# Kernel optimization log

Hardware: AMD Instinct MI355X
Metric: run time of the kernel (lower is better)

Reference implementation:

```python
import math
import jax, jax.numpy as jnp
import numpy as np

B, N, D, Pd, L, H = 2, 384, 256, 64, 8, 8
Dh = D // H
VOCAB = 21


def _layernorm(x, w, b, eps=1e-5):
    m = jnp.mean(x, axis=-1, keepdims=True)
    v = jnp.var(x, axis=-1, keepdims=True)
    return (x - m) * jax.lax.rsqrt(v + eps) * w + b


def _safe_norm(v):
    return jnp.sqrt(jnp.sum(v * v, axis=-1, keepdims=True) + 1e-8)


def _rot6d(r6):
    # Zhou et al. 6D rotation -> 3x3 via Gram-Schmidt (rows b1,b2,b3)
    a1, a2 = r6[..., :3], r6[..., 3:6]
    b1 = a1 / _safe_norm(a1)
    a2p = a2 - jnp.sum(b1 * a2, axis=-1, keepdims=True) * b1
    b2 = a2p / _safe_norm(a2p)
    b3 = jnp.cross(b1, b2)
    return jnp.stack([b1, b2, b3], axis=-2)  # [..., 3, 3]


def _pos_enc(n, d):
    pos = jnp.arange(n, dtype=jnp.float32)[:, None]
    div = jnp.exp(jnp.arange(0, d, 2, dtype=jnp.float32) * (-math.log(10000.0) / d))
    ang = pos * div  # [n, d/2]
    return jnp.zeros((n, d), jnp.float32).at[:, 0::2].set(jnp.sin(ang)).at[:, 1::2].set(jnp.cos(ang))


def _se3_frame_attention(Q, K, V, frames):
    # Frame-conditioned attention: dot-product scores biased by squared
    # distance between frame translations (IPA-style point bias).
    t = frames[..., :3, 3]                                   # [B,N,3]
    d2 = jnp.sum((t[:, :, None] - t[:, None, :]) ** 2, -1)   # [B,N,N]
    s = jnp.einsum('bihd,bjhd->bhij', Q, K) / math.sqrt(Dh) - d2[:, None]
    a = jax.nn.softmax(s, axis=-1)
    return jnp.einsum('bhij,bjhd->bihd', a, V)               # [B,N,H,Dh]


def _encode(tokens, tok_emb, emb_ln_w, emb_ln_b, Wq, Wk, Wv, Wo, bo,
            attn_ln_w, attn_ln_b, ff_ln_w, ff_ln_b, W1, b1, W2, b2,
            Wop, bop, relpos_emb, pair_ln_w, pair_ln_b, Wf1, bf1, Wf2, bf2):
    Bb, Nn = tokens.shape
    x = tok_emb[tokens] + _pos_enc(Nn, D)[None]
    x = _layernorm(x, emb_ln_w, emb_ln_b)
    frames = jnp.broadcast_to(jnp.eye(4, dtype=x.dtype), (Bb, Nn, 4, 4))
    pos = jnp.arange(Nn)
    rel = jnp.clip(pos[None, :] - pos[:, None], -64, 64) + 64  # rel[i,j]=pos[j]-pos[i]
    rel_e = relpos_emb[rel]                                    # [N,N,Pd]
    bot = jnp.broadcast_to(jnp.array([0.0, 0.0, 0.0, 1.0], x.dtype), (Bb, Nn, 1, 4))
    for l in range(L):
        # SE3 attention block (dropout = identity in eval)
        Q = (x @ Wq[l]).reshape(Bb, Nn, H, Dh)
        Kh = (x @ Wk[l]).reshape(Bb, Nn, H, Dh)
        Vh = (x @ Wv[l]).reshape(Bb, Nn, H, Dh)
        ao = _se3_frame_attention(Q, Kh, Vh, frames).reshape(Bb, Nn, D)
        x = _layernorm(x + ao @ Wo[l] + bo[l], attn_ln_w[l], attn_ln_b[l])
        # FFN (pre-LN inside the Sequential), residual add
        h = _layernorm(x, ff_ln_w[l], ff_ln_b[l])
        x = x + (jax.nn.gelu(h @ W1[l] + b1[l], approximate=False) @ W2[l] + b2[l])
        # Pair features
        proj = jax.nn.relu(x @ Wop + bop)                      # [B,N,Pd]
        pair = _layernorm(proj[:, :, None] + proj[:, None, :] + rel_e[None],
                          pair_ln_w, pair_ln_b)                # [B,N,N,Pd]
        # Frame head
        feat = jnp.concatenate([x, pair.mean(axis=2)], axis=-1)
        raw = jax.nn.silu(feat @ Wf1 + bf1) @ Wf2 + bf2        # [B,N,9]
        R = _rot6d(raw[..., :6])
        trans = raw[..., 6:]
        top = jnp.concatenate([R, trans[..., None]], axis=-1)  # [B,N,3,4]
        frames = jnp.concatenate([top, bot], axis=-2)          # [B,N,4,4]
    return frames, x


def setup_inputs() -> dict:
    key = jax.random.key(0)
    ks = iter(jax.random.split(key, 16))
    def w(shape, scale):
        return (jax.random.normal(next(ks), shape) * scale).astype(jnp.float32)
    return {
        'tokens': jax.random.randint(next(ks), (B, N), 0, VOCAB, dtype=jnp.int32),
        'tok_emb': w((VOCAB, D), 0.02),
        'emb_ln_w': jnp.ones((D,), jnp.float32), 'emb_ln_b': jnp.zeros((D,), jnp.float32),
        'Wq': w((L, D, D), D ** -0.5), 'Wk': w((L, D, D), D ** -0.5),
        'Wv': w((L, D, D), D ** -0.5), 'Wo': w((L, D, D), D ** -0.5),
        'bo': jnp.zeros((L, D), jnp.float32),
        'attn_ln_w': jnp.ones((L, D), jnp.float32), 'attn_ln_b': jnp.zeros((L, D), jnp.float32),
        'ff_ln_w': jnp.ones((L, D), jnp.float32), 'ff_ln_b': jnp.zeros((L, D), jnp.float32),
        'W1': w((L, D, 4 * D), D ** -0.5), 'b1': jnp.zeros((L, 4 * D), jnp.float32),
        'W2': w((L, 4 * D, D), (4 * D) ** -0.5), 'b2': jnp.zeros((L, D), jnp.float32),
        'Wop': w((D, Pd), D ** -0.5), 'bop': jnp.zeros((Pd,), jnp.float32),
        'relpos_emb': w((129, Pd), 0.02),
        'pair_ln_w': jnp.ones((Pd,), jnp.float32), 'pair_ln_b': jnp.zeros((Pd,), jnp.float32),
        'Wf1': w((D + Pd, 128), (D + Pd) ** -0.5), 'bf1': jnp.zeros((128,), jnp.float32),
        'Wf2': w((128, 9), 128 ** -0.5), 'bf2': jnp.zeros((9,), jnp.float32),
    }


def reference(tokens, tok_emb, emb_ln_w, emb_ln_b, Wq, Wk, Wv, Wo, bo,
              attn_ln_w, attn_ln_b, ff_ln_w, ff_ln_b, W1, b1, W2, b2,
              Wop, bop, relpos_emb, pair_ln_w, pair_ln_b, Wf1, bf1, Wf2, bf2):
    return _encode(tokens, tok_emb, emb_ln_w, emb_ln_b, Wq, Wk, Wv, Wo, bo,
                   attn_ln_w, attn_ln_b, ff_ln_w, ff_ln_b, W1, b1, W2, b2,
                   Wop, bop, relpos_emb, pair_ln_w, pair_ln_b, Wf1, bf1, Wf2, bf2)
```

## Files before the change

### kernel.cpp

```cpp
#include <hip/hip_runtime.h>
#include <hip/hip_bf16.h>
#include <math.h>

#define B_  2
#define N_  384
#define D_  256
#define PD_ 64
#define L_  8
#define H_  8
#define DH_ 32
#define GR  4
#define IT  8
#define RT_ 132

__global__ void prologue_kernel(const int* __restrict__ tokens, const float* __restrict__ tok_emb,
                                const float* __restrict__ lnw, const float* __restrict__ lnb,
                                const float* __restrict__ relpos,
                                float* __restrict__ x, float* __restrict__ frames,
                                float* __restrict__ tx, float* __restrict__ ty,
                                float* __restrict__ tz,
                                float* __restrict__ relc, float* __restrict__ relcT,
                                float* __restrict__ xz) {
  int row = blockIdx.x;
  int n = row % N_;
  int d = threadIdx.x;
  __shared__ float rbuf[256];
  __shared__ float smr;
  if (d < 16) frames[row * 16 + d] = (d == 0 || d == 5 || d == 10 || d == 15) ? 1.0f : 0.0f;
  if (d == 16) tx[row] = 0.0f;
  if (d == 17) ty[row] = 0.0f;
  if (d == 18) tz[row] = 0.0f;
  xz[(size_t)row * D_ + d] = 0.0f;
  if (row < 129 && d >= 192) {
    int lane = d & 63;
    float s = relpos[row * PD_ + lane];
    #pragma unroll
    for (int off = 32; off >= 1; off >>= 1) s += __shfl_xor(s, off, 64);
    if (lane == 0) smr = s * (1.0f / PD_);
  }
  int tok = tokens[row];
  float val = tok_emb[tok * D_ + d];
  int i = d >> 1;
  float dv = expf((float)(2 * i) * (-logf(10000.0f) / (float)D_));
  float ang = (float)n * dv;
  val += (d & 1) ? cosf(ang) : sinf(ang);
  rbuf[d] = val; __syncthreads();
  for (int s = 128; s > 0; s >>= 1) { if (d < s) rbuf[d] += rbuf[d + s]; __syncthreads(); }
  float mean = rbuf[0] / D_;
  __syncthreads();
  rbuf[d] = val * val; __syncthreads();
  for (int s = 128; s > 0; s >>= 1) { if (d < s) rbuf[d] += rbuf[d + s]; __syncthreads(); }
  float var = rbuf[0] / D_ - mean * mean;
  float r = rsqrtf(var + 1e-5f);
  x[row * D_ + d] = (val - mean) * r * lnw[d] + lnb[d];
  if (row < 129 && d < PD_) {
    float cv = relpos[row * PD_ + d] - smr;
    relc[row * PD_ + d] = cv;
    relcT[d * RT_ + row] = cv;
  }
}

__device__ __forceinline__ void qkv_unit(int bid, int tid, const float* __restrict__ x,
                                         const float* __restrict__ Wq, const float* __restrict__ Wk,
                                         const float* __restrict__ Wv,
                                         float* __restrict__ q, float* __restrict__ kt,
                                         float* __restrict__ v, float* sA) {
  int tile = bid & 3;
  int m = (bid >> 2) % 3;
  int r0 = (bid / 12) * GR;
  float* red = sA + GR * D_;
  {
    int r = tid >> 6, lane = tid & 63;
    ((float4*)(sA + r * D_))[lane] = ((const float4*)(x + (size_t)(r0 + r) * D_))[lane];
  }
  __syncthreads();
  const float* W = (m == 0) ? Wq : (m == 1) ? Wk : Wv;
  int kc = tid >> 6, c = tid & 63;
  const float* wp = W + (size_t)(kc * 64) * D_ + tile * 64 + c;
  const float* s0 = sA + kc * 64;
  float a0 = 0.f, a1 = 0.f, a2 = 0.f, a3 = 0.f;
  for (int kk = 0; kk < 64; kk += 4) {
    float w0 = wp[(size_t)kk * D_], w1 = wp[(size_t)(kk + 1) * D_];
    float w2 = wp[(size_t)(kk + 2) * D_], w3 = wp[(size_t)(kk + 3) * D_];
    float4 h0 = *(const float4*)(s0 + 0 * D_ + kk);
    float4 h1 = *(const float4*)(s0 + 1 * D_ + kk);
    float4 h2 = *(const float4*)(s0 + 2 * D_ + kk);
    float4 h3 = *(const float4*)(s0 + 3 * D_ + kk);
    a0 = fmaf(h0.x, w0, fmaf(h0.y, w1, fmaf(h0.z, w2, fmaf(h0.w, w3, a0))));
    a1 = fmaf(h1.x, w0, fmaf(h1.y, w1, fmaf(h1.z, w2, fmaf(h1.w, w3, a1))));
    a2 = fmaf(h2.x, w0, fmaf(h2.y, w1, fmaf(h2.z, w2, fmaf(h2.w, w3, a2))));
    a3 = fmaf(h3.x, w0, fmaf(h3.y, w1, fmaf(h3.z, w2, fmaf(h3.w, w3, a3))));
  }
  red[(kc * 4 + 0) * 64 + c] = a0;
  red[(kc * 4 + 1) * 64 + c] = a1;
  red[(kc * 4 + 2) * 64 + c] = a2;
  red[(kc * 4 + 3) * 64 + c] = a3;
  __syncthreads();
  int r = tid >> 6;
  float s = red[(0 * 4 + r) * 64 + c] + red[(1 * 4 + r) * 64 + c]
          + red[(2 * 4 + r) * 64 + c] + red[(3 * 4 + r) * 64 + c];
  int col = tile * 64 + c;
  int row = r0 + r;
  if (m == 1) {
    int b = row / N_, j = row % N_;
    int hh = col >> 5, dd = col & 31;
    kt[((size_t)(b * H_ + hh) * DH_ + dd) * N_ + j] = s;
  } else {
    float* O = (m == 0) ? q : v;
    O[(size_t)row * D_ + col] = s;
  }
}

__device__ __forceinline__ void proj_unit(int row, int tid, const float* __restrict__ x,
                                          const float* __restrict__ Wop, const float* __restrict__ bop,
                                          float* __restrict__ projc, float* __restrict__ projcT,
                                          float* __restrict__ zbuf, float* smem) {
  float* sA  = smem;
  float* red = smem + 256;
  zbuf[(size_t)row * D_ + tid] = 0.0f;
  if (tid < 64) ((float4*)sA)[tid] = ((const float4*)(x + (size_t)row * D_))[tid];
  __syncthreads();
  int kc = tid >> 6, c = tid & 63;
  const float* wp = Wop + (kc * 64) * PD_ + c;
  const float* s0 = sA + kc * 64;
  float a0 = 0.f, a1 = 0.f, a2 = 0.f, a3 = 0.f;
  for (int kk = 0; kk < 64; kk += 4) {
    a0 = fmaf(s0[kk],     wp[(kk)     * PD_], a0);
    a1 = fmaf(s0[kk + 1], wp[(kk + 1) * PD_], a1);
    a2 = fmaf(s0[kk + 2], wp[(kk + 2) * PD_], a2);
    a3 = fmaf(s0[kk + 3], wp[(kk + 3) * PD_], a3);
  }
  red[kc * 64 + c] = (a0 + a1) + (a2 + a3);
  __syncthreads();
  if (tid < 64) {
    float acc = fmaxf(bop[tid] + red[tid] + red[64 + tid] + red[128 + tid] + red[192 + tid], 0.0f);
    float s = acc;
    #pragma unroll
    for (int off = 32; off >= 1; off >>= 1) s += __shfl_xor(s, off, 64);
    float cv = acc - s * (1.0f / PD_);
    projc[row * PD_ + tid] = cv;
    projcT[(size_t)tid * (B_ * N_) + row] = cv;
  }
}

__global__ void qkv_kernel(const float* __restrict__ x, const float* __restrict__ Wq,
                           const float* __restrict__ Wk, const float* __restrict__ Wv,
                           float* __restrict__ q, float* __restrict__ kt, float* __restrict__ v) {
  __shared__ __align__(16) float smem[2048];
  qkv_unit(blockIdx.x, threadIdx.x, x, Wq, Wk, Wv, q, kt, v, smem);
}

__global__ void proj_qkv_kernel(const float* __restrict__ x,
                                const float* __restrict__ Wop, const float* __restrict__ bop,
                                float* __restrict__ projc, float* __restrict__ projcT,
                                const float* __restrict__ Wq, const float* __restrict__ Wk,
                                const float* __restrict__ Wv,
                                float* __restrict__ q, float* __restrict__ kt,
                                float* __restrict__ v, float* __restrict__ zbuf) {
  __shared__ __align__(16) float smem[2048];
  int bid = blockIdx.x, tid = threadIdx.x;
  if (bid < B_ * N_) proj_unit(bid, tid, x, Wop, bop, projc, projcT, zbuf, smem);
  else               qkv_unit(bid - B_ * N_, tid, x, Wq, Wk, Wv, q, kt, v, smem);
}

__global__ void ff_fused_kernel(const float* __restrict__ S, const float* __restrict__ bo,
                                const float* __restrict__ alnw, const float* __restrict__ alnb,
                                const float* __restrict__ flnw, const float* __restrict__ flnb,
                                const float* __restrict__ W1, const float* __restrict__ b1,
                                const float* __restrict__ W2, const float* __restrict__ b2v,
                                float* __restrict__ T) {
  int bid = blockIdx.x;
  int tile = bid & 7;
  int r0 = (bid >> 3) * GR;
  int tid = threadIdx.x;
  __shared__ __align__(16) float sA[GR * D_];
  __shared__ __align__(16) float sX[GR * D_];
  __shared__ float red[2 * GR * 128];
  __shared__ __align__(16) float sF[128 * 4];
  {
    int r = tid >> 6, lane = tid & 63;
    float4 v = ((const float4*)(S + (size_t)(r0 + r) * D_))[lane];
    float4 bo4 = ((const float4*)bo)[lane];
    v.x += bo4.x; v.y += bo4.y; v.z += bo4.z; v.w += bo4.w;
    float s = v.x + v.y + v.z + v.w;
    float s2 = v.x * v.x + v.y * v.y + v.z * v.z + v.w * v.w;
    #pragma unroll
    for (int off = 32; off >= 1; off >>= 1) {
      s  += __shfl_xor(s, off, 64);
      s2 += __shfl_xor(s2, off, 64);
    }
    float mean = s * (1.0f / D_);
    float var = s2 * (1.0f / D_) - mean * mean;
    float rin = rsqrtf(var + 1e-5f);
    float4 aw = ((const float4*)alnw)[lane];
    float4 ab = ((const float4*)alnb)[lane];
    float4 x4;
    x4.x = (v.x - mean) * rin * aw.x + ab.x;
    x4.y = (v.y - mean) * rin * aw.y + ab.y;
    x4.z = (v.z - mean) * rin * aw.z + ab.z;
    x4.w = (v.w - mean) * rin * aw.w + ab.w;
    ((float4*)(sX + r * D_))[lane] = x4;
    float t = x4.x + x4.y + x4.z + x4.w;
    float t2 = x4.x * x4.x + x4.y * x4.y + x4.z * x4.z + x4.w * x4.w;
    #pragma unroll
    for (int off = 32; off >= 1; off >>= 1) {
      t  += __shfl_xor(t, off, 64);
      t2 += __shfl_xor(t2, off, 64);
    }
    float mean2 = t * (1.0f / D_);
    float var2 = t2 * (1.0f / D_) - mean2 * mean2;
    float rin2 = rsqrtf(var2 + 1e-5f);
    float4 fw = ((const float4*)flnw)[lane];
    float4 fb = ((const float4*)flnb)[lane];
    float4 h4;
    h4.x = (x4.x - mean2) * rin2 * fw.x + fb.x;
    h4.y = (x4.y - mean2) * rin2 * fw.y + fb.y;
    h4.z = (x4.z - mean2) * rin2 * fw.z + fb.z;
    h4.w = (x4.w - mean2) * rin2 * fw.w + fb.w;
    ((float4*)(sA + r * D_))[lane] = h4;
  }
  __syncthreads();
  {
    int kc = tid >> 7, c = tid & 127;
    int col = tile * 128 + c;
    const float* wp = W1 + (size_t)(kc * 128) * 1024 + col;
    const float* s0 = sA + kc * 128;
    float a0 = 0.f, a1 = 0.f, a2 = 0.f, a3 = 0.f;
    for (int kk = 0; kk < 128; kk += 4) {
      float w0 = wp[(size_t)kk * 1024], w1 = wp[(size_t)(kk + 1) * 1024];
      float w2 = wp[(size_t)(kk + 2) * 1024], w3 = wp[(size_t)(kk + 3) * 1024];
      float4 h0 = *(const float4*)(s0 + 0 * D_ + kk);
      float4 h1 = *(const float4*)(s0 + 1 * D_ + kk);
      float4 h2 = *(const float4*)(s0 + 2 * D_ + kk);
      float4 h3 = *(const float4*)(s0 + 3 * D_ + kk);
      a0 = fmaf(h0.x, w0, fmaf(h0.y, w1, fmaf(h0.z, w2, fmaf(h0.w, w3, a0))));
      a1 = fmaf(h1.x, w0, fmaf(h1.y, w1, fmaf(h1.z, w2, fmaf(h1.w, w3, a1))));
      a2 = fmaf(h2.x, w0, fmaf(h2.y, w1, fmaf(h2.z, w2, fmaf(h2.w, w3, a2))));
      a3 = fmaf(h3.x, w0, fmaf(h3.y, w1, fmaf(h3.z, w2, fmaf(h3.w, w3, a3))));
    }
    red[(kc * 4 + 0) * 128 + c] = a0;
    red[(kc * 4 + 1) * 128 + c] = a1;
    red[(kc * 4 + 2) * 128 + c] = a2;
    red[(kc * 4 + 3) * 128 + c] = a3;
  }
  __syncthreads();
  {
    int rA = tid >> 7, c = tid & 127;
    int col = tile * 128 + c;
    #pragma unroll
    for (int p = 0; p < 2; p++) {
      int r = rA + p * 2;
      float s = red[(0 * 4 + r) * 128 + c] + red[(1 * 4 + r) * 128 + c] + b1[col];
      s = 0.5f * s * (1.0f + erff(s * 0.7071067811865475f));
      sF[c * 4 + r] = s;
    }
  }
  __syncthreads();
  {
    const float* w2p = W2 + (size_t)(tile * 128) * D_ + tid;
    float o0 = 0.f, o1 = 0.f, o2 = 0.f, o3 = 0.f;
    #pragma unroll 8
    for (int k = 0; k < 128; k++) {
      float w = w2p[(size_t)k * D_];
      float4 f4 = *(const float4*)(sF + k * 4);
      o0 = fmaf(f4.x, w, o0); o1 = fmaf(f4.y, w, o1);
      o2 = fmaf(f4.z, w, o2); o3 = fmaf(f4.w, w, o3);
    }
    if (tile == 0) {
      float bb2 = b2v[tid];
      o0 += sX[0 * D_ + tid] + bb2;
      o1 += sX[1 * D_ + tid] + bb2;
      o2 += sX[2 * D_ + tid] + bb2;
      o3 += sX[3 * D_ + tid] + bb2;
    }
    atomicAdd(&T[(size_t)(r0 + 0) * D_ + tid], o0);
    atomicAdd(&T[(size_t)(r0 + 1) * D_ + tid], o1);
    atomicAdd(&T[(size_t)(r0 + 2) * D_ + tid], o2);
    atomicAdd(&T[(size_t)(r0 + 3) * D_ + tid], o3);
  }
}

__global__ void attn_kernel(const float* __restrict__ Q, const float* __restrict__ KT,
                            const float* __restrict__ V,
                            const float* __restrict__ tx, const float* __restrict__ ty,
                            const float* __restrict__ tz,
                            const float* __restrict__ Wo, float* __restrict__ S) {
  const int TILES = N_ / IT;
  int bid = blockIdx.x;
  int it = bid % TILES;
  int h  = (bid / TILES) % H_;
  int b  = bid / (TILES * H_);
  int i0 = it * IT;
  int tid = threadIdx.x;
  int wave = tid >> 6, lane = tid & 63;

  __shared__ __align__(16) float sQ[IT * DH_];
  __shared__ __align__(16) float sK[DH_ * 64];
  __shared__ __align__(16) float sV[64 * DH_];
  __shared__ __align__(16) float sS[IT][N_];
  __shared__ float sti[3][IT];
  __shared__ float sinv[IT];

  {
    int ii = tid >> 5, d = tid & 31;
    sQ[ii * DH_ + d] = Q[((size_t)(b * N_ + i0 + ii)) * D_ + h * DH_ + d];
  }
  if (tid < IT) {
    sti[0][tid] = tx[b * N_ + i0 + tid];
    sti[1][tid] = ty[b * N_ + i0 + tid];
    sti[2][tid] = tz[b * N_ + i0 + tid];
  }
  const float* ktb = KT + (size_t)(b * H_ + h) * DH_ * N_;
  const float* vb  = V + (size_t)b * N_ * D_ + h * DH_;
  const float* txb = tx + b * N_;
  const float* tyb = ty + b * N_;
  const float* tzb = tz + b * N_;
  __syncthreads();

  float4 q0r[8], q1r[8];
  #pragma unroll
  for (int t = 0; t < 8; t++) {
    q0r[t] = ((const float4*)(sQ + (wave * 2 + 0) * DH_))[t];
    q1r[t] = ((const float4*)(sQ + (wave * 2 + 1) * DH_))[t];
  }

  for (int jc = 0; jc < N_; jc += 64) {
    for (int idx = tid; idx < DH_ * 64; idx += 256) {
      int d = idx >> 6, jj = idx & 63;
      sK[d * 64 + jj] = ktb[(size_t)d * N_ + jc + jj];
    }
    __syncthreads();
    int jj = lane;
    float tjx = txb[jc + jj], tjy = tyb[jc + jj], tjz = tzb[jc + jj];
    float a0 = 0.f, a1 = 0.f;
    #pragma unroll
    for (int t = 0; t < 8; t++) {
      float k0 = sK[(4 * t + 0) * 64 + jj];
      float k1 = sK[(4 * t + 1) * 64 + jj];
      float k2 = sK[(4 * t + 2) * 64 + jj];
      float k3 = sK[(4 * t + 3) * 64 + jj];
      float4 qa = q0r[t], qb = q1r[t];
      a0 = fmaf(qa.x, k0, fmaf(qa.y, k1, fmaf(qa.z, k2, fmaf(qa.w, k3, a0))));
      a1 = fmaf(qb.x, k0, fmaf(qb.y, k1, fmaf(qb.z, k2, fmaf(qb.w, k3, a1))));
    }
    #pragma unroll
    for (int s = 0; s < 2; s++) {
      int ii = wave * 2 + s;
      float a = (s == 0) ? a0 : a1;
      float dx = sti[0][ii] - tjx;
      float dy = sti[1][ii] - tjy;
      float dz = sti[2][ii] - tjz;
      sS[ii][jc + jj] = a * 0.17677669529663689f - (dx * dx + dy * dy + dz * dz);
    }
    __syncthreads();
  }

  #pragma unroll
  for (int s = 0; s < 2; s++) {
    int ii = wave * 2 + s;
    float vrow[6];
    float m = -1e30f;
    #pragma unroll
    for (int t = 0; t < 6; t++) { vrow[t] = sS[ii][t * 64 + lane]; m = fmaxf(m, vrow[t]); }
    #pragma unroll
    for (int off = 32; off >= 1; off >>= 1) m = fmaxf(m, __shfl_xor(m, off, 64));
    float ps = 0.f;
    #pragma unroll
    for (int t = 0; t < 6; t++) {
      float e = expf(vrow[t] - m);
      sS[ii][t * 64 + lane] = e;
      ps += e;
    }
    #pragma unroll
    for (int off = 32; off >= 1; off >>= 1) ps += __shfl_xor(ps, off, 64);
    if (lane == 0) sinv[ii] = 1.0f / ps;
  }
  __syncthreads();

  int ii = tid >> 5, dd = tid & 31;
  float o0 = 0.f, o1 = 0.f;
  for (int jc = 0; jc < N_; jc += 64) {
    for (int idx = tid; idx < 64 * DH_; idx += 256) {
      int jj = idx >> 5, d = idx & 31;
      sV[jj * DH_ + d] = vb[(size_t)(jc + jj) * D_ + d];
    }
    __syncthreads();
    const float* srow = &sS[ii][jc];
    #pragma unroll
    for (int jj = 0; jj < 64; jj += 4) {
      float4 sv = *(const float4*)(srow + jj);
      o0 = fmaf(sv.x, sV[(jj + 0) * DH_ + dd], o0);
      o1 = fmaf(sv.y, sV[(jj + 1) * DH_ + dd], o1);
      o0 = fmaf(sv.z, sV[(jj + 2) * DH_ + dd], o0);
      o1 = fmaf(sv.w, sV[(jj + 3) * DH_ + dd], o1);
    }
    __syncthreads();
  }

  sQ[tid] = (o0 + o1) * sinv[ii];
  __syncthreads();
  {
    const float* wo = Wo + (size_t)(h * DH_) * D_ + tid;
    float acc[8];
    #pragma unroll
    for (int r = 0; r < 8; r++) acc[r] = 0.f;
    for (int k = 0; k < DH_; k += 4) {
      float w0 = wo[(size_t)(k + 0) * D_];
      float w1 = wo[(size_t)(k + 1) * D_];
      float w2 = wo[(size_t)(k + 2) * D_];
      float w3 = wo[(size_t)(k + 3) * D_];
      #pragma unroll
      for (int r = 0; r < 8; r++) {
        float4 a4 = *(const float4*)(sQ + r * DH_ + k);
        acc[r] = fmaf(a4.x, w0, fmaf(a4.y, w1, fmaf(a4.z, w2, fmaf(a4.w, w3, acc[r]))));
      }
    }
    float* Sb = S + ((size_t)(b * N_ + i0)) * D_ + tid;
    #pragma unroll
    for (int r = 0; r < 8; r++) atomicAdd(Sb + (size_t)r * D_, acc[r]);
  }
}

__global__ void pair_head_kernel(const float* __restrict__ projc, const float* __restrict__ projcT,
                                 const float* __restrict__ relc, const float* __restrict__ relcT,
                                 const float* __restrict__ lnw, const float* __restrict__ lnb,
                                 const float* __restrict__ x,
                                 const float* __restrict__ Wf1, const float* __restrict__ bWf1,
                                 const float* __restrict__ Wf2, const float* __restrict__ bWf2,
                                 float* __restrict__ frames, float* __restrict__ tx,
                                 float* __restrict__ ty, float* __restrict__ tz) {
  const int M = B_ * N_;
  int row = blockIdx.x;
  int b = row / N_;
  int i = row % N_;
  int tid = threadIdx.x;
  int lane = tid & 63;
  int wave = tid >> 6;
  __shared__ float svpi[PD_];
  __shared__ float sr[N_];
  __shared__ float red[4][PD_];
  __shared__ float sfeat[320];
  __shared__ float fred[2][128];
  __shared__ float sg[128];
  __shared__ float sraw[9];

  if (tid < PD_) svpi[tid] = projc[row * PD_ + tid];
  if (tid < D_) sfeat[tid] = x[(size_t)row * D_ + tid];
  __syncthreads();

  {
    int jA = tid;
    int raA = jA - i; raA = raA < -64 ? -64 : (raA > 64 ? 64 : raA); raA += 64;
    const float* pA = projcT + b * N_ + jA;
    const float* rA = relcT + raA;
    float s2A = 0.f;
    #pragma unroll 8
    for (int c = 0; c < PD_; c++) {
      float dA = svpi[c] + pA[(size_t)c * M] + rA[c * RT_];
      s2A = fmaf(dA, dA, s2A);
    }
    sr[jA] = rsqrtf(s2A * (1.0f / PD_) + 1e-5f);
    if (tid < 128) {
      int jB = tid + 256;
      int raB = jB - i; raB = raB < -64 ? -64 : (raB > 64 ? 64 : raB); raB += 64;
      const float* pB = projcT + b * N_ + jB;
      const float* rB = relcT + raB;
      float s2B = 0.f;
      #pragma unroll 8
      for (int c = 0; c < PD_; c++) {
        float dB = svpi[c] + pB[(size_t)c * M] + rB[c * RT_];
        s2B = fmaf(dB, dB, s2B);
      }
      sr[jB] = rsqrtf(s2B * (1.0f / PD_) + 1e-5f);
    }
  }
  __syncthreads();

  {
    float vpl = svpi[lane];
    const float* pb = projc + (size_t)b * N_ * PD_;
    float acc = 0.0f;
    for (int j = wave * 2; j < N_; j += 8) {
      int ja = j, jb = j + 1;
      int ra = ja - i; ra = ra < -64 ? -64 : (ra > 64 ? 64 : ra); ra += 64;
      int rb = jb - i; rb = rb < -64 ? -64 : (rb > 64 ? 64 : rb); rb += 64;
      float da = vpl + pb[ja * PD_ + lane] + relc[ra * PD_ + lane];
      float db = vpl + pb[jb * PD_ + lane] + relc[rb * PD_ + lane];
      acc = fmaf(da, sr[ja], fmaf(db, sr[jb], acc));
    }
    red[wave][lane] = acc;
  }
  __syncthreads();
  if (wave == 0) {
    float s = red[0][lane] + red[1][lane] + red[2][lane] + red[3][lane];
    sfeat[D_ + lane] = lnb[lane] + s * lnw[lane] * (1.0f / N_);
  }
  __syncthreads();

  int kc = tid >> 7, c = tid & 127;
  int koff = kc * 160;
  const float* wp = Wf1 + (size_t)koff * 128 + c;
  const float* s0 = sfeat + koff;
  float a0 = 0.f, a1 = 0.f, a2 = 0.f, a3 = 0.f;
  for (int kk = 0; kk < 160; kk += 4) {
    a0 = fmaf(s0[kk],     wp[(size_t)kk * 128],       a0);
    a1 = fmaf(s0[kk + 1], wp[(size_t)(kk + 1) * 128], a1);
    a2 = fmaf(s0[kk + 2], wp[(size_t)(kk + 2) * 128], a2);
    a3 = fmaf(s0[kk + 3], wp[(size_t)(kk + 3) * 128], a3);
  }
  fred[kc][c] = (a0 + a1) + (a2 + a3);
  __syncthreads();
  if (tid < 128) {
    float g = fred[0][tid] + fred[1][tid] + bWf1[tid];
    sg[tid] = g / (1.0f + expf(-g));
  }
  __syncthreads();

  if (tid < 9) {
    float b0 = 0.f, b1v = 0.f;
    for (int kk = 0; kk < 128; kk += 2) {
      b0  = fmaf(sg[kk],     Wf2[(kk)     * 9 + tid], b0);
      b1v = fmaf(sg[kk + 1], Wf2[(kk + 1) * 9 + tid], b1v);
    }
    sraw[tid] = bWf2[tid] + b0 + b1v;
  }
  __syncthreads();
  if (tid == 0) {
    float a1x = sraw[0], a1y = sraw[1], a1z = sraw[2];
    float a2x = sraw[3], a2y = sraw[4], a2z = sraw[5];
    float n1 = sqrtf(a1x * a1x + a1y * a1y + a1z * a1z + 1e-8f);
    float b1x = a1x / n1, b1y = a1y / n1, b1z = a1z / n1;
    float dp = b1x * a2x + b1y * a2y + b1z * a2z;
    float px = a2x - dp * b1x, py = a2y - dp * b1y, pz = a2z - dp * b1z;
    float n2 = sqrtf(px * px + py * py + pz * pz + 1e-8f);
    float b2x = px / n2, b2y = py / n2, b2z = pz / n2;
    float b3x = b1y * b2z - b1z * b2y;
    float b3y = b1z * b2x - b1x * b2z;
    float b3z = b1x * b2y - b1y * b2x;
    float* f = frames + row * 16;
    f[0]  = b1x; f[1]  = b1y; f[2]  = b1z; f[3]  = sraw[6];
    f[4]  = b2x; f[5]  = b2y; f[6]  = b2z; f[7]  = sraw[7];
    f[8]  = b3x; f[9]  = b3y; f[10] = b3z; f[11] = sraw[8];
    f[12] = 0.0f; f[13] = 0.0f; f[14] = 0.0f; f[15] = 1.0f;
    tx[row] = sraw[6];
    ty[row] = sraw[7];
    tz[row] = sraw[8];
  }
}

__global__ void write_out_kernel(const float* __restrict__ frames, const float* __restrict__ x,
                                 float* __restrict__ out) {
  int i = blockIdx.x * 256 + threadIdx.x;
  const int nf = B_ * N_ * 16;
  const int total = nf + B_ * N_ * D_;
  if (i < nf) out[i] = frames[i];
  else if (i < total) out[i] = x[i - nf];
}

extern "C" void kernel_launch(void* const* d_in, const int* in_sizes, int n_in,
                              void* d_out, int out_size, void* d_ws, size_t ws_size,
                              hipStream_t stream) {
  const int*   tokens    = (const int*)  d_in[0];
  const float* tok_emb   = (const float*)d_in[1];
  const float* emb_ln_w  = (const float*)d_in[2];
  const float* emb_ln_b  = (const float*)d_in[3];
  const float* Wq        = (const float*)d_in[4];
  const float* Wk        = (const float*)d_in[5];
  const float* Wv        = (const float*)d_in[6];
  const float* Wo        = (const float*)d_in[7];
  const float* bo        = (const float*)d_in[8];
  const float* attn_ln_w = (const float*)d_in[9];
  const float* attn_ln_b = (const float*)d_in[10];
  const float* ff_ln_w   = (const float*)d_in[11];
  const float* ff_ln_b   = (const float*)d_in[12];
  const float* W1        = (const float*)d_in[13];
  const float* b1        = (const float*)d_in[14];
  const float* W2        = (const float*)d_in[15];
  const float* b2        = (const float*)d_in[16];
  const float* Wop       = (const float*)d_in[17];
  const float* bop       = (const float*)d_in[18];
  const float* relpos    = (const float*)d_in[19];
  const float* pair_ln_w = (const float*)d_in[20];
  const float* pair_ln_b = (const float*)d_in[21];
  const float* Wf1       = (const float*)d_in[22];
  const float* bWf1      = (const float*)d_in[23];
  const float* Wf2       = (const float*)d_in[24];
  const float* bWf2      = (const float*)d_in[25];

  const int M = B_ * N_;
  const int XE = M * D_;
  float* ws     = (float*)d_ws;
  float* frames = ws;
  float* projc  = frames + M * 16;
  float* projcT = projc  + M * PD_;
  float* relc   = projcT + M * PD_;
  float* relcT  = relc   + 8320;
  float* tx     = relcT  + 8448;
  float* ty     = tx     + M;
  float* tz     = ty     + M;
  float* xA     = tz     + M;
  float* xB     = xA + XE;
  float* q      = xB + XE;
  float* kt     = q  + XE;
  float* v      = kt + XE;

  prologue_kernel<<<M, 256, 0, stream>>>(tokens, tok_emb, emb_ln_w, emb_ln_b, relpos,
                                         xA, frames, tx, ty, tz, relc, relcT, xB);
  qkv_kernel<<<(M / GR) * 12, 256, 0, stream>>>(xA, Wq, Wk, Wv, q, kt, v);

  for (int l = 0; l < L_; l++) {
    float* Sin  = (l & 1) ? xB : xA;
    float* Sout = (l & 1) ? xA : xB;
    attn_kernel<<<B_ * H_ * (N_ / IT), 256, 0, stream>>>(
        q, kt, v, tx, ty, tz, Wo + (size_t)l * D_ * D_, Sin);
    ff_fused_kernel<<<(M / GR) * 8, 256, 0, stream>>>(
        Sin, bo + l * D_,
        attn_ln_w + l * D_, attn_ln_b + l * D_,
        ff_ln_w + l * D_, ff_ln_b + l * D_,
        W1 + (size_t)l * D_ * 1024, b1 + l * 1024,
        W2 + (size_t)l * 1024 * D_, b2 + l * D_, Sout);
    if (l < L_ - 1) {
      int lq = l + 1;
      proj_qkv_kernel<<<M + (M / GR) * 12, 256, 0, stream>>>(
          Sout, Wop, bop, projc, projcT,
          Wq + (size_t)lq * D_ * D_, Wk + (size_t)lq * D_ * D_, Wv + (size_t)lq * D_ * D_,
          q, kt, v, Sin);
    } else {
      proj_qkv_kernel<<<M, 256, 0, stream>>>(Sout, Wop, bop, projc, projcT,
                                             Wq, Wk, Wv, q, kt, v, Sin);
    }
    pair_head_kernel<<<M, 256, 0, stream>>>(projc, projcT, relc, relcT, pair_ln_w, pair_ln_b,
                                            Sout, Wf1, bWf1, Wf2, bWf2, frames, tx, ty, tz);
  }

  const int total = B_ * N_ * 16 + B_ * N_ * D_;
  write_out_kernel<<<(total + 255) / 256, 256, 0, stream>>>(frames, xA, (float*)d_out);
}
```

Before: 873.4 us.

## Remap attention blocks per XCD and split PV over key halves with register reuse

Block indices are remapped so the 48 query tiles of each (batch, head) pair land on the same XCD. The aim is better L2 reuse of K and V, given round-robin workgroup dispatch across 8 XCDs. The P·V loop is restructured so each thread accumulates two query rows while reusing each loaded V value, with waves split across the two halves of the key range. Partial sums are then reduced through shared memory. This halves LDS reads of V per FMA, but leaves half the waves idle on each key chunk and adds an extra reduction and barrier.

```diff
diff --git a/kernel.cpp b/kernel.cpp
--- a/kernel.cpp
+++ b/kernel.cpp
@@ -285,11 +285,13 @@
                             const float* __restrict__ tx, const float* __restrict__ ty,
                             const float* __restrict__ tz,
                             const float* __restrict__ Wo, float* __restrict__ S) {
-  const int TILES = N_ / IT;
-  int bid = blockIdx.x;
-  int it = bid % TILES;
-  int h  = (bid / TILES) % H_;
-  int b  = bid / (TILES * H_);
+  int wgid = blockIdx.x;
+  int xcd  = wgid & 7;
+  int slot = wgid >> 3;
+  int head = xcd * 2 + (slot / 48);
+  int it   = slot % 48;
+  int h = head & 7;
+  int b = head >> 3;
   int i0 = it * IT;
   int tid = threadIdx.x;
   int wave = tid >> 6, lane = tid & 63;
@@ -377,28 +379,44 @@
   }
   __syncthreads();
 
-  int ii = tid >> 5, dd = tid & 31;
-  float o0 = 0.f, o1 = 0.f;
+  int jh = wave >> 1;
+  int p  = ((wave & 1) << 1) | (lane >> 5);
+  int dd = lane & 31;
+  int rA = 2 * p, rB = 2 * p + 1;
+  float oA = 0.f, oB = 0.f;
   for (int jc = 0; jc < N_; jc += 64) {
     for (int idx = tid; idx < 64 * DH_; idx += 256) {
       int jj = idx >> 5, d = idx & 31;
       sV[jj * DH_ + d] = vb[(size_t)(jc + jj) * D_ + d];
     }
     __syncthreads();
-    const float* srow = &sS[ii][jc];
-    #pragma unroll
-    for (int jj = 0; jj < 64; jj += 4) {
-      float4 sv = *(const float4*)(srow + jj);
-      o0 = fmaf(sv.x, sV[(jj + 0) * DH_ + dd], o0);
-      o1 = fmaf(sv.y, sV[(jj + 1) * DH_ + dd], o1);
-      o0 = fmaf(sv.z, sV[(jj + 2) * DH_ + dd], o0);
-      o1 = fmaf(sv.w, sV[(jj + 3) * DH_ + dd], o1);
+    if ((jc / 192) == jh) {
+      const float* sa = sS[rA] + jc;
+      const float* sb = sS[rB] + jc;
+      #pragma unroll
+      for (int jj = 0; jj < 64; jj += 4) {
+        float4 ea = *(const float4*)(sa + jj);
+        float4 eb = *(const float4*)(sb + jj);
+        float v0 = sV[(jj + 0) * DH_ + dd];
+        float v1 = sV[(jj + 1) * DH_ + dd];
+        float v2 = sV[(jj + 2) * DH_ + dd];
+        float v3 = sV[(jj + 3) * DH_ + dd];
+        oA = fmaf(ea.x, v0, fmaf(ea.y, v1, fmaf(ea.z, v2, fmaf(ea.w, v3, oA))));
+        oB = fmaf(eb.x, v0, fmaf(eb.y, v1, fmaf(eb.z, v2, fmaf(eb.w, v3, oB))));
+      }
     }
     __syncthreads();
   }
-
-  sQ[tid] = (o0 + o1) * sinv[ii];
-  __syncthreads();
+  float* pr = sK;
+  pr[jh * 256 + rA * 32 + dd] = oA;
+  pr[jh * 256 + rB * 32 + dd] = oB;
+  __syncthreads();
+  {
+    int ii = tid >> 5;
+    sQ[tid] = (pr[tid] + pr[256 + tid]) * sinv[ii];
+  }
+  __syncthreads();
+
   {
     const float* wo = Wo + (size_t)(h * DH_) * D_ + tid;
     float acc[8];
```

New measurement: 873.0 us. About the same (-0.0%).
